# Performance work log

Measured on AMD Instinct MI355X. Metric: run time of the kernel, lower is better.

Reference implementation:

```python
import jax, jax.numpy as jnp
import numpy as np

NUM_EMB, EMB, HID, LIN = 25, 128, 1024, 1024
T, B = 256, 32

def setup_inputs() -> dict:
    key = jax.random.key(0)
    ks = jax.random.split(key, 20)
    g = lambda k, s, sc=0.02: jax.random.normal(k, s, dtype=jnp.float32) * sc
    return {
        "emb_table": g(ks[0], (NUM_EMB, EMB), 1.0),
        "W_ih0": g(ks[1], (4 * HID, EMB)),
        "W_hh0": g(ks[2], (4 * HID, HID)),
        "b_ih0": g(ks[3], (4 * HID,)),
        "b_hh0": g(ks[4], (4 * HID,)),
        "W_ih1": g(ks[5], (4 * HID, HID)),
        "W_hh1": g(ks[6], (4 * HID, HID)),
        "b_ih1": g(ks[7], (4 * HID,)),
        "b_hh1": g(ks[8], (4 * HID,)),
        "lin_W": g(ks[9], (LIN, 2 * HID)),
        "lin_b": g(ks[10], (LIN,)),
        "out_W": g(ks[11], (1, LIN)),
        "out_b": g(ks[12], (1,)),
        # tokens in [-1, NUM_EMB): -1 means padding -> zero embedding
        "tokens_L": jax.random.randint(ks[13], (T, B), -1, NUM_EMB, dtype=jnp.int32),
        "tokens_R": jax.random.randint(ks[14], (T, B), -1, NUM_EMB, dtype=jnp.int32),
        "lengths_L": jax.random.randint(ks[15], (B,), T // 2, T + 1, dtype=jnp.int32),
        "lengths_R": jax.random.randint(ks[16], (B,), T // 2, T + 1, dtype=jnp.int32),
    }

def _cell(x, h, c, Wih, Whh, bih, bhh):
    # PyTorch LSTM gate order: i, f, g, o
    gates = x @ Wih.T + h @ Whh.T + bih + bhh  # [B, 4H]
    i, f, gg, o = jnp.split(gates, 4, axis=-1)
    c2 = jax.nn.sigmoid(f) * c + jax.nn.sigmoid(i) * jnp.tanh(gg)
    h2 = jax.nn.sigmoid(o) * jnp.tanh(c2)
    return h2, c2

def _run_branch(tokens, lengths, emb_table,
                W_ih0, W_hh0, b_ih0, b_hh0, W_ih1, W_hh1, b_ih1, b_hh1):
    # masked embedding gather: -1 -> zero vector (single vectorized gather)
    valid = (tokens >= 0)
    xs = emb_table[jnp.clip(tokens, 0, NUM_EMB - 1)]  # [T, B, E]
    xs = xs * valid[..., None].astype(xs.dtype)
    Bn = xs.shape[1]

    def step(carry, inp):
        h1, c1, h2, c2 = carry
        x, t = inp
        nh1, nc1 = _cell(x, h1, c1, W_ih0, W_hh0, b_ih0, b_hh0)
        nh2, nc2 = _cell(nh1, h2, c2, W_ih1, W_hh1, b_ih1, b_hh1)
        m = (t < lengths)[:, None]  # freeze state past each seq's length (packed semantics)
        return (jnp.where(m, nh1, h1), jnp.where(m, nc1, c1),
                jnp.where(m, nh2, h2), jnp.where(m, nc2, c2)), None

    z = jnp.zeros((Bn, HID), xs.dtype)
    (h1, c1, h2, c2), _ = jax.lax.scan(step, (z, z, z, z),
                                       (xs, jnp.arange(xs.shape[0])))
    return h2  # last-layer final hidden, == h_n[-1]

def reference(emb_table, W_ih0, W_hh0, b_ih0, b_hh0, W_ih1, W_hh1, b_ih1, b_hh1,
              lin_W, lin_b, out_W, out_b, tokens_L, tokens_R, lengths_L, lengths_R):
    hL = _run_branch(tokens_L, lengths_L, emb_table,
                     W_ih0, W_hh0, b_ih0, b_hh0, W_ih1, W_hh1, b_ih1, b_hh1)
    hR = _run_branch(tokens_R, lengths_R, emb_table,
                     W_ih0, W_hh0, b_ih0, b_hh0, W_ih1, W_hh1, b_ih1, b_hh1)
    h = jnp.concatenate([hL, hR], axis=1)          # [B, 2H]
    h = jax.nn.relu(h @ lin_W.T + lin_b)            # [B, LIN]
    out = h @ out_W.T + out_b                        # [B, 1]
    return out.reshape(-1)
```

## Files before the change

### kernel.cpp

```cpp
#include <hip/hip_runtime.h>


typedef _Float16 h16;
typedef h16  h16x8 __attribute__((ext_vector_type(8)));
typedef float f32x4 __attribute__((ext_vector_type(4)));

#define NWG 256
#define WGT 1024

#define OFF_IHB   ((size_t)0)
#define OFF_H1    ((size_t)425984)
#define OFF_H2    ((size_t)688128)
#define OFF_SYNC  ((size_t)950272)
#define ZERO_OFF  OFF_H1
#define ZERO_BYTES ((size_t)(262144 + 262144 + 262144))

#define LDS_WB    98304
#define LDS_SCRF  10752
#define LDS_TOTAL (LDS_WB + 43008 + 1664)

#define LDG_SC(dst, base, OFFB)                                          \
  asm volatile("global_load_dwordx4 %0, %1, off offset:" #OFFB " sc0 sc1" \
               : "=v"(dst) : "v"(base))

__device__ __forceinline__ void stg_sc_h16(h16* p, float v) {
  union { h16 h; unsigned short u; } cv;
  cv.h = (h16)v;
  unsigned vv = cv.u;
  asm volatile("global_store_short %0, %1, off sc0 sc1"
               :: "v"(p), "v"(vv) : "memory");
}

__device__ __forceinline__ float sigm(float x) {
  return 1.0f / (1.0f + __expf(-x));
}
__device__ __forceinline__ float tanh_(float x) {
  float e = __expf(2.0f * x);
  return 1.0f - 2.0f / (e + 1.0f);
}

__global__ void __launch_bounds__(64) prep_ihb(
    const float* __restrict__ emb, const float* __restrict__ wih0,
    const float* __restrict__ bih0, const float* __restrict__ bhh0,
    float* __restrict__ ihb) {
  int g = blockIdx.x / 26, e = blockIdx.x % 26;
  int l = threadIdx.x, c = l & 15, q = l >> 4;
  int gate = c & 3, jj = c >> 2;
  int row = (gate << 10) + (g << 2) + jj;
  float s = 0.f;
  if (e < 25) {
    const float* er = emb + e * 128 + q * 32;
    const float* wr = wih0 + row * 128 + q * 32;
#pragma unroll
    for (int k = 0; k < 32; k += 4) {
      float4 a = *(const float4*)(er + k);
      float4 b = *(const float4*)(wr + k);
      s += a.x * b.x + a.y * b.y + a.z * b.z + a.w * b.w;
    }
  }
  s += __shfl_xor(s, 16);
  s += __shfl_xor(s, 32);
  if (q == 0) ihb[(g * 26 + e) * 16 + c] = s + bih0[row] + bhh0[row];
}

__device__ __forceinline__ void gbar(unsigned* syncb, int p) {
  asm volatile("s_waitcnt vmcnt(0)" ::: "memory");
  __syncthreads();
  if (threadIdx.x == 0) {
    unsigned* base = syncb + (size_t)p * 256;
    const int grp = (int)(blockIdx.x >> 5);
    if (__hip_atomic_fetch_add(base + grp * 4, 1u, __ATOMIC_RELAXED,
                               __HIP_MEMORY_SCOPE_AGENT) == 31u) {
      if (__hip_atomic_fetch_add(base + 8 * 4, 1u, __ATOMIC_RELAXED,
                                 __HIP_MEMORY_SCOPE_AGENT) == 7u) {
        __hip_atomic_store(base + 15 * 4, 1u, __ATOMIC_RELAXED,
                           __HIP_MEMORY_SCOPE_AGENT);
      }
    }
    while (__hip_atomic_load(base + 15 * 4, __ATOMIC_RELAXED,
                             __HIP_MEMORY_SCOPE_AGENT) == 0u) {
      __builtin_amdgcn_s_sleep(1);
    }
  }
  __syncthreads();
  asm volatile("" ::: "memory");
}


__global__ void __launch_bounds__(WGT, 1) lstm_main(
    const float* __restrict__ whh0, const float* __restrict__ wih1,
    const float* __restrict__ whh1, const float* __restrict__ ihb,
    const float* __restrict__ bih1, const float* __restrict__ bhh1,
    h16* __restrict__ h1buf, h16* __restrict__ h2buf,
    unsigned* __restrict__ syncb,
    const int* __restrict__ tokL, const int* __restrict__ tokR,
    const int* __restrict__ lenL, const int* __restrict__ lenR) {
  extern __shared__ char lds[];
  h16* wlds = (h16*)lds;
  float* scr = (float*)(lds + LDS_WB);
  float* ihbL = scr + LDS_SCRF;
  const int g = (int)blockIdx.x;
  const int tid = (int)threadIdx.x;
  const int w = tid >> 6, lane = tid & 63;
  const int rg = w & 3, kq = w >> 2;
  const int bl = lane & 15, hi = lane >> 4;

  for (int ch = tid; ch < 6144; ch += WGT) {
    int m = ch >> 11, rem = ch & 2047, kk = rem >> 6, ln = rem & 63;
    int c = ln & 15, lh = ln >> 4;
    int rowW = ((c & 3) << 10) + (g << 2) + (c >> 2);
    const float* src =
        (m == 0 ? whh0 : (m == 1 ? wih1 : whh1)) + rowW * 1024 + kk * 32 + lh * 8;
    float4 v0 = *(const float4*)(src);
    float4 v1 = *(const float4*)(src + 4);
    h16x8 o;
    o[0] = (h16)v0.x; o[1] = (h16)v0.y; o[2] = (h16)v0.z; o[3] = (h16)v0.w;
    o[4] = (h16)v1.x; o[5] = (h16)v1.y; o[6] = (h16)v1.z; o[7] = (h16)v1.w;
    *(h16x8*)(wlds + (size_t)ch * 8) = o;
  }
  for (int i = tid; i < 416; i += WGT) ihbL[i] = ihb[g * 416 + i];
  __syncthreads();

  const int mR = lane & 15, jjF = lane >> 4;
  const int rgF = w & 3;
  const int rowF = rgF * 16 + mR;
  const int bF = (rowF < 32) ? rowF : rowF - 32;
  const int* tokF = (rowF < 32) ? tokL : tokR;
  const int lenF = (rowF < 32) ? lenL[bF] : lenR[bF];
  const int jglob = (g << 2) + jjF;
  f32x4 bb;
#pragma unroll
  for (int q = 0; q < 4; ++q) {
    int rowW = q * 1024 + (g << 2) + jjF;
    bb[q] = bih1[rowW] + bhh1[rowW];
  }

  float c1 = 0.f, h1v = 0.f, c2 = 0.f, h2v = 0.f;

  for (int p = 0; p <= 256; ++p) {
    const int r = p & 1;
    const h16* a1p = h1buf + r * 65536 + (rg * 16 + bl) * 1024 + kq * 256 + hi * 8;
    const h16* a2p = h2buf + (r ^ 1) * 65536 + (rg * 16 + bl) * 1024 + kq * 256 + hi * 8;
    f32x4 A1r[8], A2r[8];
    LDG_SC(A1r[0], a1p, 0);   LDG_SC(A1r[1], a1p, 64);
    LDG_SC(A1r[2], a1p, 128); LDG_SC(A1r[3], a1p, 192);
    LDG_SC(A1r[4], a1p, 256); LDG_SC(A1r[5], a1p, 320);
    LDG_SC(A1r[6], a1p, 384); LDG_SC(A1r[7], a1p, 448);
    LDG_SC(A2r[0], a2p, 0);   LDG_SC(A2r[1], a2p, 64);
    LDG_SC(A2r[2], a2p, 128); LDG_SC(A2r[3], a2p, 192);
    LDG_SC(A2r[4], a2p, 256); LDG_SC(A2r[5], a2p, 320);
    LDG_SC(A2r[6], a2p, 384); LDG_SC(A2r[7], a2p, 448);

    int e = 25;
    if (w < 4 && p < 256) {
      int tok = tokF[p * 32 + bF];
      e = (tok < 0) ? 25 : tok;
    }

    asm volatile("s_waitcnt vmcnt(0)" ::: "memory");
    __builtin_amdgcn_sched_barrier(0);

    f32x4 acc0 = {0.f, 0.f, 0.f, 0.f};
    f32x4 acca = {0.f, 0.f, 0.f, 0.f};
    f32x4 accb = {0.f, 0.f, 0.f, 0.f};
#pragma unroll
    for (int i = 0; i < 8; ++i) {
      int kk = kq * 8 + i;
      h16x8 a1 = __builtin_bit_cast(h16x8, A1r[i]);
      h16x8 a2 = __builtin_bit_cast(h16x8, A2r[i]);
      h16x8 b0 = *(const h16x8*)(wlds + ((size_t)(0 * 32 + kk) * 64 + lane) * 8);
      h16x8 b1 = *(const h16x8*)(wlds + ((size_t)(1 * 32 + kk) * 64 + lane) * 8);
      h16x8 b2 = *(const h16x8*)(wlds + ((size_t)(2 * 32 + kk) * 64 + lane) * 8);
      acc0 = __builtin_amdgcn_mfma_f32_16x16x32_f16(a1, b0, acc0, 0, 0, 0);
      acca = __builtin_amdgcn_mfma_f32_16x16x32_f16(a1, b1, acca, 0, 0, 0);
      accb = __builtin_amdgcn_mfma_f32_16x16x32_f16(a2, b2, accb, 0, 0, 0);
    }
    f32x4 s1 = acca + accb;

#pragma unroll
    for (int q = 0; q < 4; ++q) {
      int m = (hi << 2) + q;
      scr[((0 + rg) * 16 + m) * 84 + kq * 21 + bl] = acc0[q];
      scr[((4 + rg) * 16 + m) * 84 + kq * 21 + bl] = s1[q];
    }
    __syncthreads();

    if (w < 8) {
      const bool cell0 = (w < 4);
      if ((cell0 && p < 256) || (!cell0 && p >= 1)) {
        const float* sb = scr + ((size_t)w * 16 + mR) * 84 + (jjF << 2);
        f32x4 gv = {0.f, 0.f, 0.f, 0.f};
#pragma unroll
        for (int k2 = 0; k2 < 4; ++k2) gv += *(const f32x4*)(sb + k2 * 21);
        if (cell0) {
          f32x4 ib = *(const f32x4*)(ihbL + (e << 4) + (jjF << 2));
          float gi = gv[0] + ib[0], gf = gv[1] + ib[1];
          float gg = gv[2] + ib[2], go = gv[3] + ib[3];
          if (p < lenF) {
            float iv = sigm(gi), fv = sigm(gf), gt = tanh_(gg), ov = sigm(go);
            c1 = fv * c1 + iv * gt;
            h1v = ov * tanh_(c1);
          }
          stg_sc_h16(h1buf + (r ^ 1) * 65536 + rowF * 1024 + jglob, h1v);
        } else {
          float gi = gv[0] + bb[0], gf = gv[1] + bb[1];
          float gg = gv[2] + bb[2], go = gv[3] + bb[3];
          if (p - 1 < lenF) {
            float iv = sigm(gi), fv = sigm(gf), gt = tanh_(gg), ov = sigm(go);
            c2 = fv * c2 + iv * gt;
            h2v = ov * tanh_(c2);
          }
          stg_sc_h16(h2buf + r * 65536 + rowF * 1024 + jglob, h2v);
        }
      }
    }

    if (p < 256) gbar(syncb, p);
  }
}


__global__ void __launch_bounds__(256) head_kernel(
    const h16* __restrict__ h2, const float* __restrict__ linW,
    const float* __restrict__ linb, const float* __restrict__ outW,
    const float* __restrict__ outb, float* __restrict__ out) {
  __shared__ h16 hl[2048];
  __shared__ float red[4];
  const int b = (int)blockIdx.x >> 2, lq = (int)blockIdx.x & 3;
  const int tid = (int)threadIdx.x;
  {
    int k0 = tid * 8;
    const h16* src = (k0 < 1024) ? (h2 + b * 1024 + k0)
                                 : (h2 + (b + 32) * 1024 + (k0 - 1024));
    *(h16x8*)(hl + k0) = *(const h16x8*)src;
  }
  __syncthreads();
  const int l = lq * 256 + tid;
  float acc = linb[l];
  const float* wr = linW + (size_t)l * 2048;
  for (int k = 0; k < 2048; k += 4) {
    float4 wv = *(const float4*)(wr + k);
    acc += wv.x * (float)hl[k] + wv.y * (float)hl[k + 1] +
           wv.z * (float)hl[k + 2] + wv.w * (float)hl[k + 3];
  }
  float v = fmaxf(acc, 0.f) * outW[l];
  for (int off = 32; off > 0; off >>= 1) v += __shfl_down(v, off);
  if ((tid & 63) == 0) red[tid >> 6] = v;
  __syncthreads();
  if (tid == 0) {
    float s = red[0] + red[1] + red[2] + red[3];
    if (lq == 0) s += outb[0];
    atomicAdd(out + b, s);
  }
}


extern "C" void kernel_launch(void* const* d_in, const int* in_sizes, int n_in,
                              void* d_out, int out_size, void* d_ws,
                              size_t ws_size, hipStream_t stream) {
  (void)in_sizes; (void)n_in; (void)out_size; (void)ws_size;
  const float* emb  = (const float*)d_in[0];
  const float* wih0 = (const float*)d_in[1];
  const float* whh0 = (const float*)d_in[2];
  const float* bih0 = (const float*)d_in[3];
  const float* bhh0 = (const float*)d_in[4];
  const float* wih1 = (const float*)d_in[5];
  const float* whh1 = (const float*)d_in[6];
  const float* bih1 = (const float*)d_in[7];
  const float* bhh1 = (const float*)d_in[8];
  const float* linW = (const float*)d_in[9];
  const float* linb = (const float*)d_in[10];
  const float* outW = (const float*)d_in[11];
  const float* outb = (const float*)d_in[12];
  const int* tokL = (const int*)d_in[13];
  const int* tokR = (const int*)d_in[14];
  const int* lenL = (const int*)d_in[15];
  const int* lenR = (const int*)d_in[16];

  char* ws = (char*)d_ws;
  float* IHBp    = (float*)(ws + OFF_IHB);
  h16* H1p       = (h16*)(ws + OFF_H1);
  h16* H2p       = (h16*)(ws + OFF_H2);
  unsigned* SYp  = (unsigned*)(ws + OFF_SYNC);

  hipMemsetAsync(ws + ZERO_OFF, 0, ZERO_BYTES, stream);
  hipMemsetAsync(d_out, 0, 32 * sizeof(float), stream);

  prep_ihb<<<6656, 64, 0, stream>>>(emb, wih0, bih0, bhh0, IHBp);

  hipFuncSetAttribute((const void*)lstm_main,
                      hipFuncAttributeMaxDynamicSharedMemorySize, LDS_TOTAL);
  void* kargs[] = {(void*)&whh0, (void*)&wih1, (void*)&whh1, (void*)&IHBp,
                   (void*)&bih1, (void*)&bhh1, (void*)&H1p,  (void*)&H2p,
                   (void*)&SYp,  (void*)&tokL, (void*)&tokR, (void*)&lenL,
                   (void*)&lenR};
  hipLaunchCooperativeKernel((const void*)lstm_main, dim3(NWG), dim3(WGT),
                             kargs, (unsigned)LDS_TOTAL, stream);

  head_kernel<<<128, 256, 0, stream>>>(H2p, linW, linb, outW, outb,
                                       (float*)d_out);
}
```

Measured before the change: 3.764 ms.

## Split LSTM layers across dedicated workgroups with 512-thread blocks

```diff
diff --git a/kernel.cpp b/kernel.cpp
--- a/kernel.cpp
+++ b/kernel.cpp
@@ -6,7 +6,7 @@
 typedef float f32x4 __attribute__((ext_vector_type(4)));
 
 #define NWG 256
-#define WGT 1024
+#define WGT 512
 
 #define OFF_IHB   ((size_t)0)
 #define OFF_H1    ((size_t)425984)
@@ -15,9 +15,10 @@
 #define ZERO_OFF  OFF_H1
 #define ZERO_BYTES ((size_t)(262144 + 262144 + 262144))
 
-#define LDS_WB    98304
-#define LDS_SCRF  10752
-#define LDS_TOTAL (LDS_WB + 43008 + 1664)
+#define LDS_WOFF  0
+#define LDS_SOFF  131072
+#define LDS_IOFF  (131072 + 18432)
+#define LDS_TOTAL (131072 + 18432 + 3328)
 
 #define LDG_SC(dst, base, OFFB)                                          \
   asm volatile("global_load_dwordx4 %0, %1, off offset:" #OFFB " sc0 sc1" \
@@ -44,23 +45,22 @@
     const float* __restrict__ bih0, const float* __restrict__ bhh0,
     float* __restrict__ ihb) {
   int g = blockIdx.x / 26, e = blockIdx.x % 26;
-  int l = threadIdx.x, c = l & 15, q = l >> 4;
+  int l = threadIdx.x, c = l & 31, q = l >> 5;
   int gate = c & 3, jj = c >> 2;
-  int row = (gate << 10) + (g << 2) + jj;
+  int row = (gate << 10) + g * 8 + jj;
   float s = 0.f;
   if (e < 25) {
-    const float* er = emb + e * 128 + q * 32;
-    const float* wr = wih0 + row * 128 + q * 32;
-#pragma unroll
-    for (int k = 0; k < 32; k += 4) {
+    const float* er = emb + e * 128 + q * 64;
+    const float* wr = wih0 + row * 128 + q * 64;
+#pragma unroll
+    for (int k = 0; k < 64; k += 4) {
       float4 a = *(const float4*)(er + k);
       float4 b = *(const float4*)(wr + k);
       s += a.x * b.x + a.y * b.y + a.z * b.z + a.w * b.w;
     }
   }
-  s += __shfl_xor(s, 16);
   s += __shfl_xor(s, 32);
-  if (q == 0) ihb[(g * 26 + e) * 16 + c] = s + bih0[row] + bhh0[row];
+  if (q == 0) ihb[(g * 26 + e) * 32 + c] = s + bih0[row] + bhh0[row];
 }
 
 __device__ __forceinline__ void gbar(unsigned* syncb, int p) {
@@ -87,7 +87,7 @@
 }
 
 
-__global__ void __launch_bounds__(WGT, 1) lstm_main(
+__global__ void __launch_bounds__(WGT, 2) lstm_main(
     const float* __restrict__ whh0, const float* __restrict__ wih1,
     const float* __restrict__ whh1, const float* __restrict__ ihb,
     const float* __restrict__ bih1, const float* __restrict__ bhh1,
@@ -96,21 +96,24 @@
     const int* __restrict__ tokL, const int* __restrict__ tokR,
     const int* __restrict__ lenL, const int* __restrict__ lenR) {
   extern __shared__ char lds[];
-  h16* wlds = (h16*)lds;
-  float* scr = (float*)(lds + LDS_WB);
-  float* ihbL = scr + LDS_SCRF;
-  const int g = (int)blockIdx.x;
+  h16* wlds = (h16*)(lds + LDS_WOFF);
+  float* scr = (float*)(lds + LDS_SOFF);
+  float* ihbL = (float*)(lds + LDS_IOFF);
+  const int bid = (int)blockIdx.x;
+  const int role = bid >> 7;
+  const int og = bid & 127;
   const int tid = (int)threadIdx.x;
-  const int w = tid >> 6, lane = tid & 63;
-  const int rg = w & 3, kq = w >> 2;
+  const int wv = tid >> 6, lane = tid & 63;
+  const int rg = wv & 3, kq = wv >> 2;
   const int bl = lane & 15, hi = lane >> 4;
 
-  for (int ch = tid; ch < 6144; ch += WGT) {
-    int m = ch >> 11, rem = ch & 2047, kk = rem >> 6, ln = rem & 63;
-    int c = ln & 15, lh = ln >> 4;
-    int rowW = ((c & 3) << 10) + (g << 2) + (c >> 2);
-    const float* src =
-        (m == 0 ? whh0 : (m == 1 ? wih1 : whh1)) + rowW * 1024 + kk * 32 + lh * 8;
+  const int nch = role ? 8192 : 4096;
+  for (int ch = tid; ch < nch; ch += WGT) {
+    int m = ch >> 12, nt = (ch >> 11) & 1, kk = (ch >> 6) & 31, ln = ch & 63;
+    int c = nt * 16 + (ln & 15), ksub = ln >> 4;
+    int row = ((c & 3) << 10) + og * 8 + (c >> 2);
+    const float* wsrc = role ? (m ? whh1 : wih1) : whh0;
+    const float* src = wsrc + row * 1024 + kk * 32 + ksub * 8;
     float4 v0 = *(const float4*)(src);
     float4 v1 = *(const float4*)(src + 4);
     h16x8 o;
@@ -118,41 +121,58 @@
     o[4] = (h16)v1.x; o[5] = (h16)v1.y; o[6] = (h16)v1.z; o[7] = (h16)v1.w;
     *(h16x8*)(wlds + (size_t)ch * 8) = o;
   }
-  for (int i = tid; i < 416; i += WGT) ihbL[i] = ihb[g * 416 + i];
-  __syncthreads();
-
-  const int mR = lane & 15, jjF = lane >> 4;
-  const int rgF = w & 3;
-  const int rowF = rgF * 16 + mR;
+  if (!role) {
+    for (int i = tid; i < 832; i += WGT) ihbL[i] = ihb[og * 832 + i];
+  }
+  __syncthreads();
+
+  const int rowF = lane;
+  const int jF = wv;
   const int bF = (rowF < 32) ? rowF : rowF - 32;
   const int* tokF = (rowF < 32) ? tokL : tokR;
   const int lenF = (rowF < 32) ? lenL[bF] : lenR[bF];
-  const int jglob = (g << 2) + jjF;
-  f32x4 bb;
-#pragma unroll
-  for (int q = 0; q < 4; ++q) {
-    int rowW = q * 1024 + (g << 2) + jjF;
-    bb[q] = bih1[rowW] + bhh1[rowW];
-  }
-
-  float c1 = 0.f, h1v = 0.f, c2 = 0.f, h2v = 0.f;
+  const int jglob = og * 8 + jF;
+  f32x4 bb = {0.f, 0.f, 0.f, 0.f};
+  if (role) {
+#pragma unroll
+    for (int q = 0; q < 4; ++q) {
+      int row = (q << 10) + jglob;
+      bb[q] = bih1[row] + bhh1[row];
+    }
+  }
+
+  float cs = 0.f, hv = 0.f;
 
   for (int p = 0; p <= 256; ++p) {
     const int r = p & 1;
-    const h16* a1p = h1buf + r * 65536 + (rg * 16 + bl) * 1024 + kq * 256 + hi * 8;
-    const h16* a2p = h2buf + (r ^ 1) * 65536 + (rg * 16 + bl) * 1024 + kq * 256 + hi * 8;
-    f32x4 A1r[8], A2r[8];
-    LDG_SC(A1r[0], a1p, 0);   LDG_SC(A1r[1], a1p, 64);
-    LDG_SC(A1r[2], a1p, 128); LDG_SC(A1r[3], a1p, 192);
-    LDG_SC(A1r[4], a1p, 256); LDG_SC(A1r[5], a1p, 320);
-    LDG_SC(A1r[6], a1p, 384); LDG_SC(A1r[7], a1p, 448);
-    LDG_SC(A2r[0], a2p, 0);   LDG_SC(A2r[1], a2p, 64);
-    LDG_SC(A2r[2], a2p, 128); LDG_SC(A2r[3], a2p, 192);
-    LDG_SC(A2r[4], a2p, 256); LDG_SC(A2r[5], a2p, 320);
-    LDG_SC(A2r[6], a2p, 384); LDG_SC(A2r[7], a2p, 448);
+    const size_t abase = (size_t)(rg * 16 + bl) * 1024 + kq * 512 + hi * 8;
+    const h16* a1p = h1buf + r * 65536 + abase;
+
+    f32x4 A1r[16];
+    LDG_SC(A1r[0],  a1p, 0);   LDG_SC(A1r[1],  a1p, 64);
+    LDG_SC(A1r[2],  a1p, 128); LDG_SC(A1r[3],  a1p, 192);
+    LDG_SC(A1r[4],  a1p, 256); LDG_SC(A1r[5],  a1p, 320);
+    LDG_SC(A1r[6],  a1p, 384); LDG_SC(A1r[7],  a1p, 448);
+    LDG_SC(A1r[8],  a1p, 512); LDG_SC(A1r[9],  a1p, 576);
+    LDG_SC(A1r[10], a1p, 640); LDG_SC(A1r[11], a1p, 704);
+    LDG_SC(A1r[12], a1p, 768); LDG_SC(A1r[13], a1p, 832);
+    LDG_SC(A1r[14], a1p, 896); LDG_SC(A1r[15], a1p, 960);
+
+    f32x4 A2r[16];
+    if (role) {
+      const h16* a2p = h2buf + (r ^ 1) * 65536 + abase;
+      LDG_SC(A2r[0],  a2p, 0);   LDG_SC(A2r[1],  a2p, 64);
+      LDG_SC(A2r[2],  a2p, 128); LDG_SC(A2r[3],  a2p, 192);
+      LDG_SC(A2r[4],  a2p, 256); LDG_SC(A2r[5],  a2p, 320);
+      LDG_SC(A2r[6],  a2p, 384); LDG_SC(A2r[7],  a2p, 448);
+      LDG_SC(A2r[8],  a2p, 512); LDG_SC(A2r[9],  a2p, 576);
+      LDG_SC(A2r[10], a2p, 640); LDG_SC(A2r[11], a2p, 704);
+      LDG_SC(A2r[12], a2p, 768); LDG_SC(A2r[13], a2p, 832);
+      LDG_SC(A2r[14], a2p, 896); LDG_SC(A2r[15], a2p, 960);
+    }
 
     int e = 25;
-    if (w < 4 && p < 256) {
+    if (!role && p < 256) {
       int tok = tokF[p * 32 + bF];
       e = (tok < 0) ? 25 : tok;
     }
@@ -160,58 +180,68 @@
     asm volatile("s_waitcnt vmcnt(0)" ::: "memory");
     __builtin_amdgcn_sched_barrier(0);
 
-    f32x4 acc0 = {0.f, 0.f, 0.f, 0.f};
-    f32x4 acca = {0.f, 0.f, 0.f, 0.f};
-    f32x4 accb = {0.f, 0.f, 0.f, 0.f};
-#pragma unroll
-    for (int i = 0; i < 8; ++i) {
-      int kk = kq * 8 + i;
-      h16x8 a1 = __builtin_bit_cast(h16x8, A1r[i]);
-      h16x8 a2 = __builtin_bit_cast(h16x8, A2r[i]);
-      h16x8 b0 = *(const h16x8*)(wlds + ((size_t)(0 * 32 + kk) * 64 + lane) * 8);
-      h16x8 b1 = *(const h16x8*)(wlds + ((size_t)(1 * 32 + kk) * 64 + lane) * 8);
-      h16x8 b2 = *(const h16x8*)(wlds + ((size_t)(2 * 32 + kk) * 64 + lane) * 8);
-      acc0 = __builtin_amdgcn_mfma_f32_16x16x32_f16(a1, b0, acc0, 0, 0, 0);
-      acca = __builtin_amdgcn_mfma_f32_16x16x32_f16(a1, b1, acca, 0, 0, 0);
-      accb = __builtin_amdgcn_mfma_f32_16x16x32_f16(a2, b2, accb, 0, 0, 0);
-    }
-    f32x4 s1 = acca + accb;
-
-#pragma unroll
-    for (int q = 0; q < 4; ++q) {
-      int m = (hi << 2) + q;
-      scr[((0 + rg) * 16 + m) * 84 + kq * 21 + bl] = acc0[q];
-      scr[((4 + rg) * 16 + m) * 84 + kq * 21 + bl] = s1[q];
-    }
+    f32x4 acc[2];
+    acc[0] = f32x4{0.f, 0.f, 0.f, 0.f};
+    acc[1] = f32x4{0.f, 0.f, 0.f, 0.f};
+    if (role) {
+#pragma unroll
+      for (int kk = 0; kk < 16; ++kk) {
+        int kabs = kq * 16 + kk;
+        h16x8 a1 = __builtin_bit_cast(h16x8, A1r[kk]);
+        h16x8 a2 = __builtin_bit_cast(h16x8, A2r[kk]);
+#pragma unroll
+        for (int nt = 0; nt < 2; ++nt) {
+          h16x8 bi = *(const h16x8*)(wlds + ((size_t)((0 * 2 + nt) * 32 + kabs) * 64 + lane) * 8);
+          h16x8 bh = *(const h16x8*)(wlds + ((size_t)((1 * 2 + nt) * 32 + kabs) * 64 + lane) * 8);
+          acc[nt] = __builtin_amdgcn_mfma_f32_16x16x32_f16(a1, bi, acc[nt], 0, 0, 0);
+          acc[nt] = __builtin_amdgcn_mfma_f32_16x16x32_f16(a2, bh, acc[nt], 0, 0, 0);
+        }
+      }
+    } else {
+#pragma unroll
+      for (int kk = 0; kk < 16; ++kk) {
+        int kabs = kq * 16 + kk;
+        h16x8 a1 = __builtin_bit_cast(h16x8, A1r[kk]);
+#pragma unroll
+        for (int nt = 0; nt < 2; ++nt) {
+          h16x8 b0 = *(const h16x8*)(wlds + ((size_t)(nt * 32 + kabs) * 64 + lane) * 8);
+          acc[nt] = __builtin_amdgcn_mfma_f32_16x16x32_f16(a1, b0, acc[nt], 0, 0, 0);
+        }
+      }
+    }
+
+#pragma unroll
+    for (int nt = 0; nt < 2; ++nt)
+#pragma unroll
+      for (int q = 0; q < 4; ++q)
+        scr[(kq * 64 + rg * 16 + hi * 4 + q) * 36 + nt * 16 + bl] = acc[nt][q];
     __syncthreads();
 
-    if (w < 8) {
-      const bool cell0 = (w < 4);
-      if ((cell0 && p < 256) || (!cell0 && p >= 1)) {
-        const float* sb = scr + ((size_t)w * 16 + mR) * 84 + (jjF << 2);
-        f32x4 gv = {0.f, 0.f, 0.f, 0.f};
-#pragma unroll
-        for (int k2 = 0; k2 < 4; ++k2) gv += *(const f32x4*)(sb + k2 * 21);
-        if (cell0) {
-          f32x4 ib = *(const f32x4*)(ihbL + (e << 4) + (jjF << 2));
-          float gi = gv[0] + ib[0], gf = gv[1] + ib[1];
-          float gg = gv[2] + ib[2], go = gv[3] + ib[3];
-          if (p < lenF) {
-            float iv = sigm(gi), fv = sigm(gf), gt = tanh_(gg), ov = sigm(go);
-            c1 = fv * c1 + iv * gt;
-            h1v = ov * tanh_(c1);
-          }
-          stg_sc_h16(h1buf + (r ^ 1) * 65536 + rowF * 1024 + jglob, h1v);
-        } else {
-          float gi = gv[0] + bb[0], gf = gv[1] + bb[1];
-          float gg = gv[2] + bb[2], go = gv[3] + bb[3];
-          if (p - 1 < lenF) {
-            float iv = sigm(gi), fv = sigm(gf), gt = tanh_(gg), ov = sigm(go);
-            c2 = fv * c2 + iv * gt;
-            h2v = ov * tanh_(c2);
-          }
-          stg_sc_h16(h2buf + r * 65536 + rowF * 1024 + jglob, h2v);
-        }
+    const bool act = role ? (p >= 1) : (p < 256);
+    if (act) {
+      const float* sb = scr + rowF * 36 + (jF << 2);
+      f32x4 gv = *(const f32x4*)(sb) + *(const f32x4*)(sb + 64 * 36);
+      float gi, gf, gg, go;
+      int tcur;
+      if (!role) {
+        const f32x4 ib = *(const f32x4*)(ihbL + (e << 5) + (jF << 2));
+        gi = gv[0] + ib[0]; gf = gv[1] + ib[1];
+        gg = gv[2] + ib[2]; go = gv[3] + ib[3];
+        tcur = p;
+      } else {
+        gi = gv[0] + bb[0]; gf = gv[1] + bb[1];
+        gg = gv[2] + bb[2]; go = gv[3] + bb[3];
+        tcur = p - 1;
+      }
+      if (tcur < lenF) {
+        float iv = sigm(gi), fv = sigm(gf), gt = tanh_(gg), ov = sigm(go);
+        cs = fv * cs + iv * gt;
+        hv = ov * tanh_(cs);
+      }
+      if (!role) {
+        stg_sc_h16(h1buf + (r ^ 1) * 65536 + rowF * 1024 + jglob, hv);
+      } else {
+        stg_sc_h16(h2buf + r * 65536 + rowF * 1024 + jglob, hv);
       }
     }
 
@@ -286,7 +316,7 @@
   hipMemsetAsync(ws + ZERO_OFF, 0, ZERO_BYTES, stream);
   hipMemsetAsync(d_out, 0, 32 * sizeof(float), stream);
 
-  prep_ihb<<<6656, 64, 0, stream>>>(emb, wih0, bih0, bhh0, IHBp);
+  prep_ihb<<<3328, 64, 0, stream>>>(emb, wih0, bih0, bhh0, IHBp);
 
   hipFuncSetAttribute((const void*)lstm_main,
                       hipFuncAttributeMaxDynamicSharedMemorySize, LDS_TOTAL);
```

New measurement: 3.717 ms. No clear change (-1.3%).
